# Performance work log

Measured on AMD Instinct MI355X. Metric: run time of the kernel, lower is better.

The kernel has to match this reference:

```python
import jax, jax.numpy as jnp
import numpy as np
import math

MARGIN = 0.5
SCALE = 64.0
CURVATURE = 1.0
COS_M = math.cos(MARGIN)
SIN_M = math.sin(MARGIN)
TH = math.cos(math.pi - MARGIN)
MM = math.sin(math.pi - MARGIN) * MARGIN

B, D, C = 2048, 512, 16384


def setup_inputs() -> dict:
    key = jax.random.key(0)
    k1, k2, k3 = jax.random.split(key, 3)
    embeddings = jax.random.normal(k1, (B, D), dtype=jnp.float32) * 0.05  # roughly inside the ball
    labels = jax.random.randint(k2, (B,), 0, C)
    # xavier_uniform for [C, D]
    limit = math.sqrt(6.0 / (C + D))
    weight = jax.random.uniform(k3, (C, D), dtype=jnp.float32, minval=-limit, maxval=limit)
    return {"embeddings": embeddings, "labels": labels, "weight": weight}


def _exp_map_zero(v, c):
    sqrt_c = c ** 0.5
    v_norm = jnp.maximum(jnp.linalg.norm(v, axis=-1, keepdims=True), 1e-7)
    return jnp.tanh(sqrt_c * v_norm) * v / (sqrt_c * v_norm)


def reference(embeddings, labels, weight):
    c = CURVATURE
    # class prototypes mapped onto the Poincare ball, clipped to radius 0.95
    proto = _exp_map_zero(weight, c)                                  # [C, D]
    proto_norm = jnp.linalg.norm(proto, axis=-1, keepdims=True)
    proto = jnp.where(proto_norm > 0.95, proto * 0.95 / proto_norm, proto)

    x = embeddings                                                     # [B, D]
    x_sq = jnp.sum(x * x, axis=-1)                                    # [B]
    y_sq = jnp.sum(proto * proto, axis=-1)                            # [C]
    xy = x @ proto.T                                                  # [B, C]
    diff_sq = jnp.maximum(x_sq[:, None] + y_sq[None, :] - 2.0 * xy, 0.0)

    x_sq_c = jnp.minimum(x_sq, 1.0 - 1e-5)
    y_sq_c = jnp.minimum(y_sq, 1.0 - 1e-5)
    denom = (1.0 - c * x_sq_c)[:, None] * (1.0 - c * y_sq_c)[None, :]
    arg = 1.0 + 2.0 * c * diff_sq / jnp.maximum(denom, 1e-7)
    dists = jnp.arccosh(jnp.maximum(arg, 1.0 + 1e-7)) / (c ** 0.5)    # [B, C]

    sims = jnp.exp(-dists)
    cosine = jnp.clip(2.0 * sims - 1.0, -1.0, 1.0)
    sine = jnp.sqrt(jnp.maximum(1.0 - cosine * cosine, 1e-7))
    phi = cosine * COS_M - sine * SIN_M
    phi = jnp.where(cosine > TH, phi, cosine - MM)

    one_hot = jax.nn.one_hot(labels, cosine.shape[1], dtype=cosine.dtype)
    logits = (one_hot * phi + (1.0 - one_hot) * cosine) * SCALE        # [B, C]

    logp = jax.nn.log_softmax(logits, axis=-1)
    loss = -jnp.mean(jnp.take_along_axis(logp, labels[:, None], axis=1))
    return loss
```

## Files before the change

### kernel.cpp

```cpp
#include <hip/hip_runtime.h>
#include <hip/hip_cooperative_groups.h>
#include <math.h>

namespace cg = cooperative_groups;

#define Bn 2048
#define Dn 512
#define Cn 16384

typedef float v4f __attribute__((ext_vector_type(4)));

#define WAIT_VM4()  asm volatile("s_waitcnt vmcnt(4)" ::: "memory")
#define WAIT_VM0()  asm volatile("s_waitcnt vmcnt(0)" ::: "memory")
#define RAW_BAR()   asm volatile("s_barrier" ::: "memory")
#define LGKM0_BAR() asm volatile("s_waitcnt lgkmcnt(0)\n\ts_barrier" ::: "memory")

__device__ __forceinline__ void async16(const void* g, void* l) {
  __builtin_amdgcn_global_load_lds(
      (const __attribute__((address_space(1))) char*)g,
      (__attribute__((address_space(3))) char*)l, 16, 0, 0);
}


__device__ __forceinline__ void prep_row(
    int row, int lane, const float* __restrict__ w, const float* __restrict__ x,
    char* __restrict__ wq8, char* __restrict__ xq8,
    float* __restrict__ fscale, float* __restrict__ ysqA, float* __restrict__ yrA,
    float* __restrict__ xsA, float* __restrict__ xrA)
{
  bool isW = row < Cn;
  const float* src = isW ? (w + (size_t)row * Dn) : (x + (size_t)(row - Cn) * Dn);
  const float4* s4 = (const float4*)src;
  float4 a = s4[lane * 2], b = s4[lane * 2 + 1];
  float ss = a.x * a.x + a.y * a.y + a.z * a.z + a.w * a.w
           + b.x * b.x + b.y * b.y + b.z * b.z + b.w * b.w;
  #pragma unroll
  for (int d = 1; d < 64; d <<= 1) ss += __shfl_xor(ss, d);

  int w0 = __builtin_amdgcn_cvt_pk_fp8_f32(a.x * 16.f, a.y * 16.f, 0, false);
  w0     = __builtin_amdgcn_cvt_pk_fp8_f32(a.z * 16.f, a.w * 16.f, w0, true);
  int w1 = __builtin_amdgcn_cvt_pk_fp8_f32(b.x * 16.f, b.y * 16.f, 0, false);
  w1     = __builtin_amdgcn_cvt_pk_fp8_f32(b.z * 16.f, b.w * 16.f, w1, true);
  char* dst = isW ? (wq8 + (size_t)row * Dn) : (xq8 + (size_t)(row - Cn) * Dn);
  ((int2*)dst)[lane] = make_int2(w0, w1);

  if (lane == 0) {
    if (isW) {
      float n = fmaxf(sqrtf(ss), 1e-7f);
      float t = tanhf(n);
      float tc = fminf(t, 0.95f);
      fscale[row] = tc / n;
      float ys = tc * tc;
      ysqA[row] = ys;
      yrA[row] = 1.f / (1.f - fminf(ys, 1.f - 1e-5f));
    } else {
      int r = row - Cn;
      xsA[r] = ss;
      xrA[r] = 1.f / (1.f - fminf(ss, 1.f - 1e-5f));
    }
  }
}

__device__ __forceinline__ void gemm_job(
    int job, int tid, char* lds,
    const char* __restrict__ xq8, const char* __restrict__ wq8,
    const float* __restrict__ fscale, const float* __restrict__ ysqA,
    const float* __restrict__ yrA, const float* __restrict__ xsA,
    const float* __restrict__ xrA, float* __restrict__ partials)
{
  const int xcd = job & 7;
  const int loc = job >> 3;
  const int mt  = loc & 15;
  const int nt  = (xcd << 4) | (loc >> 4);
  const int mBase = mt * 128;
  const int nBase = nt * 128;
  const int lane = tid & 63;
  const int wv = tid >> 6;
  const int quad = lane >> 4;
  const int l16 = lane & 15;
  const int waveM = wv >> 1;
  const int waveN = wv & 1;

  v4f acc[4][4];
  #pragma unroll
  for (int i = 0; i < 4; ++i)
    #pragma unroll
    for (int j = 0; j < 4; ++j)
      acc[i][j] = (v4f){0.f, 0.f, 0.f, 0.f};

  const int s0 = tid, s1 = tid + 256;
  const int r0 = s0 >> 2, c0 = (s0 & 3) ^ ((r0 >> 1) & 3);
  const int r1 = s1 >> 2, c1 = (s1 & 3) ^ ((r1 >> 1) & 3);
  const char* gA0 = xq8 + (size_t)(mBase + r0) * Dn + c0 * 16;
  const char* gA1 = xq8 + (size_t)(mBase + r1) * Dn + c1 * 16;
  const char* gW0 = wq8 + (size_t)(nBase + r0) * Dn + c0 * 16;
  const char* gW1 = wq8 + (size_t)(nBase + r1) * Dn + c1 * 16;
  const int lo0 = s0 * 16, lo1 = s1 * 16;

  const int kx = (l16 >> 1) & 3;
  int aoff[2], boff[2];
  #pragma unroll
  for (int s = 0; s < 2; ++s) {
    int chunk = (2 * s + (quad >> 1)) ^ kx;
    aoff[s] = (waveM * 64 + l16) * 64 + chunk * 16 + (quad & 1) * 8;
    boff[s] = (waveN * 64 + l16) * 64 + chunk * 16 + (quad & 1) * 8;
  }

  #pragma unroll
  for (int t = 0; t < 2; ++t) {
    char* Ab = lds + t * 16384;
    char* Wb = Ab + 8192;
    async16(gA0 + t * 64, Ab + lo0);
    async16(gA1 + t * 64, Ab + lo1);
    async16(gW0 + t * 64, Wb + lo0);
    async16(gW1 + t * 64, Wb + lo1);
  }

  #pragma unroll
  for (int kt = 0; kt < 8; ++kt) {
    const int cur = kt & 1;
    if (kt < 7) { WAIT_VM4(); } else { WAIT_VM0(); }
    RAW_BAR();
    char* Ab = lds + cur * 16384;
    char* Wb = Ab + 8192;
    long af[4][2], bf[4][2];
    #pragma unroll
    for (int s = 0; s < 2; ++s) {
      #pragma unroll
      for (int i = 0; i < 4; ++i) af[i][s] = *(const long*)(Ab + aoff[s] + i * 1024);
      #pragma unroll
      for (int j = 0; j < 4; ++j) bf[j][s] = *(const long*)(Wb + boff[s] + j * 1024);
    }
    #pragma unroll
    for (int s = 0; s < 2; ++s)
      #pragma unroll
      for (int i = 0; i < 4; ++i)
        #pragma unroll
        for (int j = 0; j < 4; ++j)
          acc[i][j] = __builtin_amdgcn_mfma_f32_16x16x32_fp8_fp8(af[i][s], bf[j][s], acc[i][j], 0, 0, 0);
    LGKM0_BAR();
    if (kt + 2 < 8) {
      async16(gA0 + (kt + 2) * 64, Ab + lo0);
      async16(gA1 + (kt + 2) * 64, Ab + lo1);
      async16(gW0 + (kt + 2) * 64, Wb + lo0);
      async16(gW1 + (kt + 2) * 64, Wb + lo1);
    }
  }

  float ysqj[4], yrj[4], gj[4];
  #pragma unroll
  for (int j = 0; j < 4; ++j) {
    int col = nBase + waveN * 64 + j * 16 + l16;
    gj[j] = -2.f * fscale[col] * (1.f / 256.f);
    ysqj[j] = ysqA[col];
    yrj[j] = yrA[col];
  }
  #pragma unroll
  for (int i = 0; i < 4; ++i) {
    #pragma unroll
    for (int r = 0; r < 4; ++r) {
      int row = mBase + waveM * 64 + i * 16 + quad * 4 + r;
      float xs = xsA[row];
      float xr2 = 2.f * xrA[row];
      float partial = 0.f;
      if (xs >= 0.99999f) {
        #pragma unroll
        for (int j = 0; j < 4; ++j) {
          float d = fmaxf(fmaf(gj[j], acc[i][j][r], xs + ysqj[j]), 0.f);
          float z = fmaf(d, xr2 * yrj[j], 1.f);
          float u = 64.f * __builtin_amdgcn_rcpf(z);
          partial += fmaf(u, fmaf(0.5f, u, 1.f), 1.f);
        }
      } else {
        #pragma unroll
        for (int j = 0; j < 4; ++j) {
          float d = fmaxf(fmaf(gj[j], acc[i][j][r], xs + ysqj[j]), 0.f);
          float z = fmaf(d, xr2 * yrj[j], 1.f);
          float sq = sqrtf(fmaf(z, z, -1.f));
          float u = 128.f * __builtin_amdgcn_rcpf(z + sq);
          partial += __expf(u);
        }
      }
      partial += __shfl_xor(partial, 1);
      partial += __shfl_xor(partial, 2);
      partial += __shfl_xor(partial, 4);
      partial += __shfl_xor(partial, 8);
      if (l16 == 0) partials[(size_t)row * 256 + nt * 2 + waveN] = partial;
    }
  }
}

__device__ __forceinline__ float final_row_term(
    int row, int lane,
    const float* __restrict__ x, const float* __restrict__ w,
    const int* __restrict__ labels, const float* __restrict__ fscale,
    const float* __restrict__ ysqA, const float* __restrict__ yrA,
    const float* __restrict__ xsA, const float* __restrict__ xrA,
    const float* __restrict__ partials)
{
  const float* pr = partials + (size_t)row * 256;
  float sum = pr[lane] + pr[lane + 64] + pr[lane + 128] + pr[lane + 192];

  int lab = labels[row];
  const float4* xv = (const float4*)(x + (size_t)row * Dn);
  const float4* wv4 = (const float4*)(w + (size_t)lab * Dn);
  float4 a0 = xv[lane * 2], a1 = xv[lane * 2 + 1];
  float4 b0 = wv4[lane * 2], b1 = wv4[lane * 2 + 1];
  float dot = a0.x * b0.x + a0.y * b0.y + a0.z * b0.z + a0.w * b0.w
            + a1.x * b1.x + a1.y * b1.y + a1.z * b1.z + a1.w * b1.w;
  #pragma unroll
  for (int d = 1; d < 64; d <<= 1) {
    sum += __shfl_xor(sum, d);
    dot += __shfl_xor(dot, d);
  }

  float term = 0.f;
  if (lane == 0) {
    float xy = fscale[lab] * dot;
    float diff = fmaxf(xsA[row] + ysqA[lab] - 2.f * xy, 0.f);
    float z = fmaf(2.f * diff, xrA[row] * yrA[lab], 1.f);
    float sq = sqrtf(fmaf(z, z, -1.f));
    float sims = 1.f / (z + sq);
    float u_lab = 128.f * sims;
    float cosv = fmaf(2.f, sims, -1.f);
    float sine = sqrtf(fmaxf(fmaf(-cosv, cosv, 1.f), 1e-7f));
    float phi = (cosv > -0.8775825619f)
                    ? (cosv * 0.8775825619f - sine * 0.4794255386f)
                    : (cosv - 0.2397127693f);
    float e_lab = __expf(u_lab);
    float e_phi = __expf(fminf(64.f * phi + 64.f, 80.f));
    term = logf(sum - e_lab + e_phi) - 64.f * phi - 64.f;
  }
  return term;
}

__global__ __launch_bounds__(256, 3) void fused_kernel(
    const float* __restrict__ w, const float* __restrict__ x,
    const int* __restrict__ labels,
    char* __restrict__ wq8, char* __restrict__ xq8,
    float* __restrict__ fscale, float* __restrict__ ysqA, float* __restrict__ yrA,
    float* __restrict__ xsA, float* __restrict__ xrA,
    float* __restrict__ partials, float* __restrict__ terms, float* __restrict__ out)
{
  __shared__ int4 ldsv[2048];
  char* lds = (char*)ldsv;
  cg::grid_group grid = cg::this_grid();
  const int tid = threadIdx.x, lane = tid & 63, wv = tid >> 6;
  const int G = gridDim.x;
  const int gwv = (blockIdx.x << 2) | wv;
  const int wavesTotal = G << 2;

  for (int row = gwv; row < Cn + Bn; row += wavesTotal)
    prep_row(row, lane, w, x, wq8, xq8, fscale, ysqA, yrA, xsA, xrA);
  grid.sync();

  #pragma unroll 1
  for (int job = blockIdx.x; job < 2048; job += G)
    gemm_job(job, tid, lds, xq8, wq8, fscale, ysqA, yrA, xsA, xrA, partials);
  grid.sync();

  {
    float mysum = 0.f;
    for (int row = gwv; row < Bn; row += wavesTotal)
      mysum += final_row_term(row, lane, x, w, labels, fscale, ysqA, yrA, xsA, xrA, partials);
    float* red = (float*)lds;
    if (lane == 0) red[wv] = mysum;
    __syncthreads();
    if (tid == 0) terms[blockIdx.x] = red[0] + red[1] + red[2] + red[3];
  }
  grid.sync();

  if (blockIdx.x == 0) {
    float a = 0.f;
    for (int i = tid; i < G; i += 256) a += terms[i];
    #pragma unroll
    for (int d = 1; d < 64; d <<= 1) a += __shfl_xor(a, d);
    float* red = (float*)lds;
    if (lane == 0) red[wv] = a;
    __syncthreads();
    if (tid == 0) out[0] = (red[0] + red[1] + red[2] + red[3]) * (1.f / (float)Bn);
  }
}

__global__ __launch_bounds__(256) void prep_kernel(
    const float* __restrict__ w, const float* __restrict__ x,
    char* __restrict__ wq8, char* __restrict__ xq8,
    float* __restrict__ fscale, float* __restrict__ ysqA, float* __restrict__ yrA,
    float* __restrict__ xsA, float* __restrict__ xrA)
{
  int row = (blockIdx.x * 256 + threadIdx.x) >> 6;
  prep_row(row, threadIdx.x & 63, w, x, wq8, xq8, fscale, ysqA, yrA, xsA, xrA);
}

__global__ __launch_bounds__(256, 3) void gemm_kernel(
    const char* __restrict__ xq8, const char* __restrict__ wq8,
    const float* __restrict__ fscale, const float* __restrict__ ysqA,
    const float* __restrict__ yrA, const float* __restrict__ xsA,
    const float* __restrict__ xrA, float* __restrict__ partials)
{
  __shared__ int4 ldsv[2048];
  gemm_job(blockIdx.x, threadIdx.x, (char*)ldsv, xq8, wq8, fscale, ysqA, yrA, xsA, xrA, partials);
}

__global__ __launch_bounds__(256) void final_kernel(
    const float* __restrict__ x, const float* __restrict__ w,
    const int* __restrict__ labels, const float* __restrict__ fscale,
    const float* __restrict__ ysqA, const float* __restrict__ yrA,
    const float* __restrict__ xsA, const float* __restrict__ xrA,
    const float* __restrict__ partials, float* __restrict__ out)
{
  int row = blockIdx.x * 4 + (threadIdx.x >> 6);
  float term = final_row_term(row, threadIdx.x & 63, x, w, labels, fscale,
                              ysqA, yrA, xsA, xrA, partials);
  __shared__ float red[4];
  if ((threadIdx.x & 63) == 0) red[threadIdx.x >> 6] = term;
  __syncthreads();
  if (threadIdx.x == 0)
    atomicAdd(out, (red[0] + red[1] + red[2] + red[3]) * (1.f / (float)Bn));
}

extern "C" void kernel_launch(void* const* d_in, const int* in_sizes, int n_in,
                              void* d_out, int out_size, void* d_ws, size_t ws_size,
                              hipStream_t stream) {
  (void)in_sizes; (void)n_in; (void)out_size; (void)ws_size;
  const float* emb = (const float*)d_in[0];
  const int* labels = (const int*)d_in[1];
  const float* weight = (const float*)d_in[2];
  float* out = (float*)d_out;

  char* p = (char*)d_ws;
  char* wq8 = p; p += (size_t)Cn * Dn;
  char* xq8 = p; p += (size_t)Bn * Dn;
  float* fscale = (float*)p; p += (size_t)Cn * 4;
  float* ysqA  = (float*)p; p += (size_t)Cn * 4;
  float* yrA   = (float*)p; p += (size_t)Cn * 4;
  float* xsA   = (float*)p; p += (size_t)Bn * 4;
  float* xrA   = (float*)p; p += (size_t)Bn * 4;
  float* partials = (float*)p; p += (size_t)Bn * 256 * 4;
  float* terms = (float*)p; p += 768 * 4;

  int dev = 0;
  hipGetDevice(&dev);
  int coopAttr = 0;
  hipDeviceGetAttribute(&coopAttr, hipDeviceAttributeCooperativeLaunch, dev);
  int maxPerCU = 0;
  hipOccupancyMaxActiveBlocksPerMultiprocessor(&maxPerCU, (const void*)fused_kernel, 256, 0);

  hipError_t le = hipErrorUnknown;
  if (coopAttr == 1 && maxPerCU >= 2) {
    int perCU = maxPerCU < 3 ? maxPerCU : 3;
    dim3 grid(256 * perCU);
    void* args[] = {(void*)&weight, (void*)&emb, (void*)&labels,
                    (void*)&wq8, (void*)&xq8, (void*)&fscale, (void*)&ysqA,
                    (void*)&yrA, (void*)&xsA, (void*)&xrA,
                    (void*)&partials, (void*)&terms, (void*)&out};
    le = hipLaunchCooperativeKernel((const void*)fused_kernel, grid, dim3(256),
                                    args, 0, stream);
  }
  if (le != hipSuccess) {
    hipMemsetAsync(out, 0, sizeof(float), stream);
    prep_kernel<<<(Cn + Bn) / 4, 256, 0, stream>>>(weight, emb, wq8, xq8, fscale, ysqA, yrA, xsA, xrA);
    gemm_kernel<<<(Bn / 128) * (Cn / 128), 256, 0, stream>>>(
        xq8, wq8, fscale, ysqA, yrA, xsA, xrA, partials);
    final_kernel<<<Bn / 4, 256, 0, stream>>>(emb, weight, labels, fscale, ysqA, yrA, xsA, xrA, partials, out);
  }
}
```

Measured before the change: 123.6 us.

## Prefetch prep rows, drop final grid sync via atomic, fast tanh, larger grid

The prep loop now software-prefetches the next row's loads before converting the current row. The last grid-wide barrier and the separate reduction block are replaced by a per-block atomicAdd into the output, which is zeroed by a memset before launch. tanhf is replaced by an exp/rcp formula, and the cooperative grid cap rises from 3 to 5 blocks per CU. This removes one grid sync and some latency at the cost of nondeterministic float summation order and an extra memset launch. Launch bounds still say 3, so occupancy may cap the grid anyway.

```diff
diff --git a/kernel.cpp b/kernel.cpp
--- a/kernel.cpp
+++ b/kernel.cpp
@@ -22,16 +22,23 @@
 }
 
 
-__device__ __forceinline__ void prep_row(
+__device__ __forceinline__ void prep_load(
     int row, int lane, const float* __restrict__ w, const float* __restrict__ x,
+    float4& a, float4& b)
+{
+  const float* src = (row < Cn) ? (w + (size_t)row * Dn) : (x + (size_t)(row - Cn) * Dn);
+  const float4* s4 = (const float4*)src;
+  a = s4[lane * 2];
+  b = s4[lane * 2 + 1];
+}
+
+__device__ __forceinline__ void prep_row_vals(
+    int row, int lane, float4 a, float4 b,
     char* __restrict__ wq8, char* __restrict__ xq8,
     float* __restrict__ fscale, float* __restrict__ ysqA, float* __restrict__ yrA,
     float* __restrict__ xsA, float* __restrict__ xrA)
 {
   bool isW = row < Cn;
-  const float* src = isW ? (w + (size_t)row * Dn) : (x + (size_t)(row - Cn) * Dn);
-  const float4* s4 = (const float4*)src;
-  float4 a = s4[lane * 2], b = s4[lane * 2 + 1];
   float ss = a.x * a.x + a.y * a.y + a.z * a.z + a.w * a.w
            + b.x * b.x + b.y * b.y + b.z * b.z + b.w * b.w;
   #pragma unroll
@@ -47,7 +54,8 @@
   if (lane == 0) {
     if (isW) {
       float n = fmaxf(sqrtf(ss), 1e-7f);
-      float t = tanhf(n);
+      float e2 = __expf(2.f * fminf(n, 10.f));
+      float t = (e2 - 1.f) * __builtin_amdgcn_rcpf(e2 + 1.f);
       float tc = fminf(t, 0.95f);
       fscale[row] = tc / n;
       float ys = tc * tc;
@@ -240,7 +248,7 @@
     char* __restrict__ wq8, char* __restrict__ xq8,
     float* __restrict__ fscale, float* __restrict__ ysqA, float* __restrict__ yrA,
     float* __restrict__ xsA, float* __restrict__ xrA,
-    float* __restrict__ partials, float* __restrict__ terms, float* __restrict__ out)
+    float* __restrict__ partials, float* __restrict__ out)
 {
   __shared__ int4 ldsv[2048];
   char* lds = (char*)ldsv;
@@ -250,8 +258,19 @@
   const int gwv = (blockIdx.x << 2) | wv;
   const int wavesTotal = G << 2;
 
-  for (int row = gwv; row < Cn + Bn; row += wavesTotal)
-    prep_row(row, lane, w, x, wq8, xq8, fscale, ysqA, yrA, xsA, xrA);
+  {
+    const int total = Cn + Bn;
+    int row = gwv;
+    float4 a = make_float4(0.f, 0.f, 0.f, 0.f), b = a;
+    if (row < total) prep_load(row, lane, w, x, a, b);
+    while (row < total) {
+      int nrow = row + wavesTotal;
+      float4 na = a, nb = b;
+      if (nrow < total) prep_load(nrow, lane, w, x, na, nb);
+      prep_row_vals(row, lane, a, b, wq8, xq8, fscale, ysqA, yrA, xsA, xrA);
+      a = na; b = nb; row = nrow;
+    }
+  }
   grid.sync();
 
   #pragma unroll 1
@@ -259,26 +278,15 @@
     gemm_job(job, tid, lds, xq8, wq8, fscale, ysqA, yrA, xsA, xrA, partials);
   grid.sync();
 
-  {
+  if (blockIdx.x * 4 < Bn) {
     float mysum = 0.f;
     for (int row = gwv; row < Bn; row += wavesTotal)
       mysum += final_row_term(row, lane, x, w, labels, fscale, ysqA, yrA, xsA, xrA, partials);
     float* red = (float*)lds;
     if (lane == 0) red[wv] = mysum;
     __syncthreads();
-    if (tid == 0) terms[blockIdx.x] = red[0] + red[1] + red[2] + red[3];
-  }
-  grid.sync();
-
-  if (blockIdx.x == 0) {
-    float a = 0.f;
-    for (int i = tid; i < G; i += 256) a += terms[i];
-    #pragma unroll
-    for (int d = 1; d < 64; d <<= 1) a += __shfl_xor(a, d);
-    float* red = (float*)lds;
-    if (lane == 0) red[wv] = a;
-    __syncthreads();
-    if (tid == 0) out[0] = (red[0] + red[1] + red[2] + red[3]) * (1.f / (float)Bn);
+    if (tid == 0)
+      atomicAdd(out, (red[0] + red[1] + red[2] + red[3]) * (1.f / (float)Bn));
   }
 }
 
@@ -289,7 +297,10 @@
     float* __restrict__ xsA, float* __restrict__ xrA)
 {
   int row = (blockIdx.x * 256 + threadIdx.x) >> 6;
-  prep_row(row, threadIdx.x & 63, w, x, wq8, xq8, fscale, ysqA, yrA, xsA, xrA);
+  int lane = threadIdx.x & 63;
+  float4 a, b;
+  prep_load(row, lane, w, x, a, b);
+  prep_row_vals(row, lane, a, b, wq8, xq8, fscale, ysqA, yrA, xsA, xrA);
 }
 
 __global__ __launch_bounds__(256, 3) void gemm_kernel(
@@ -337,7 +348,8 @@
   float* xsA   = (float*)p; p += (size_t)Bn * 4;
   float* xrA   = (float*)p; p += (size_t)Bn * 4;
   float* partials = (float*)p; p += (size_t)Bn * 256 * 4;
-  float* terms = (float*)p; p += 768 * 4;
+
+  hipMemsetAsync(out, 0, sizeof(float), stream);
 
   int dev = 0;
   hipGetDevice(&dev);
@@ -348,17 +360,16 @@
 
   hipError_t le = hipErrorUnknown;
   if (coopAttr == 1 && maxPerCU >= 2) {
-    int perCU = maxPerCU < 3 ? maxPerCU : 3;
+    int perCU = maxPerCU < 5 ? maxPerCU : 5;
     dim3 grid(256 * perCU);
     void* args[] = {(void*)&weight, (void*)&emb, (void*)&labels,
                     (void*)&wq8, (void*)&xq8, (void*)&fscale, (void*)&ysqA,
                     (void*)&yrA, (void*)&xsA, (void*)&xrA,
-                    (void*)&partials, (void*)&terms, (void*)&out};
+                    (void*)&partials, (void*)&out};
     le = hipLaunchCooperativeKernel((const void*)fused_kernel, grid, dim3(256),
                                     args, 0, stream);
   }
   if (le != hipSuccess) {
-    hipMemsetAsync(out, 0, sizeof(float), stream);
     prep_kernel<<<(Cn + Bn) / 4, 256, 0, stream>>>(weight, emb, wq8, xq8, fscale, ysqA, yrA, xsA, xrA);
     gemm_kernel<<<(Bn / 128) * (Cn / 128), 256, 0, stream>>>(
         xq8, wq8, fscale, ysqA, yrA, xsA, xrA, partials);
```

After: 125.2 us. About the same (+1.3%).
